# Optimization experiments

Hardware: AMD Instinct MI355X
Metric: run time of the kernel (lower is better)

## Reference

```python
import jax, jax.numpy as jnp
import numpy as np

N = 16_777_216
EPS = 1e-6  # keep probabilities strictly inside (0,1) so log terms are finite


def setup_inputs() -> dict:
    key = jax.random.key(0)
    k1, k2 = jax.random.split(key)
    inputs = jax.random.uniform(k1, (N,), dtype=jnp.float32, minval=EPS, maxval=1.0 - EPS)
    targets = jax.random.randint(k2, (N,), 0, 2, dtype=jnp.int32)
    return {"inputs": inputs, "targets": targets}


def reference(inputs, targets):
    t = targets.astype(inputs.dtype)
    # multiplier = 1.0 + 0.1 per element with prediction > 0.5 but label 0
    # (vectorized equivalent of the original per-element Python loop)
    count = jnp.sum(((inputs > 0.5) & (targets == 0)).astype(inputs.dtype))
    multiplier = 1.0 + 0.1 * count
    # element-wise BCE: -(t*log(p) + (1-t)*log(1-p))
    loss = -(t * jnp.log(inputs) + (1.0 - t) * jnp.log(1.0 - inputs))
    return loss.mean() * multiplier
```

## Files before the change

kernel.cpp:

```cpp
#include <hip/hip_runtime.h>


#define N_ELEM  16777216
#define N_VEC4  (N_ELEM / 4)
#define BLOCKS  2048
#define TPB     256
#define NTHREAD (BLOCKS * TPB)
#define NITER   (N_VEC4 / NTHREAD)

typedef float f4v __attribute__((ext_vector_type(4)));
typedef int   i4v __attribute__((ext_vector_type(4)));


__global__ __launch_bounds__(TPB, 4) void cl_reduce(
    const f4v* __restrict__ p4,
    const i4v* __restrict__ t4,
    float2*    __restrict__ part)
{
    const int tid = blockIdx.x * TPB + threadIdx.x;

    f4v p[NITER];
    i4v t[NITER];
    #pragma unroll
    for (int j = 0; j < NITER; ++j) {
        p[j] = __builtin_nontemporal_load(&p4[tid + j * NTHREAD]);
        t[j] = __builtin_nontemporal_load(&t4[tid + j * NTHREAD]);
    }
    __builtin_amdgcn_sched_barrier(0);

    float        lsum = 0.0f;
    unsigned int lcnt = 0u;
    #pragma unroll
    for (int j = 0; j < NITER; ++j) {
        lsum += __logf(t[j][0] ? p[j][0] : 1.0f - p[j][0]);
        lsum += __logf(t[j][1] ? p[j][1] : 1.0f - p[j][1]);
        lsum += __logf(t[j][2] ? p[j][2] : 1.0f - p[j][2]);
        lsum += __logf(t[j][3] ? p[j][3] : 1.0f - p[j][3]);
        lcnt += (unsigned int)((p[j][0] > 0.5f) & (t[j][0] == 0));
        lcnt += (unsigned int)((p[j][1] > 0.5f) & (t[j][1] == 0));
        lcnt += (unsigned int)((p[j][2] > 0.5f) & (t[j][2] == 0));
        lcnt += (unsigned int)((p[j][3] > 0.5f) & (t[j][3] == 0));
    }
    lsum = -lsum;

    #pragma unroll
    for (int off = 32; off > 0; off >>= 1) {
        lsum += __shfl_down(lsum, off);
        lcnt += __shfl_down(lcnt, off);
    }

    __shared__ float        s_sum[4];
    __shared__ unsigned int s_cnt[4];
    const int wave = threadIdx.x >> 6;
    const int lane = threadIdx.x & 63;
    if (lane == 0) { s_sum[wave] = lsum; s_cnt[wave] = lcnt; }
    __syncthreads();
    if (threadIdx.x == 0) {
        float2 v;
        v.x = s_sum[0] + s_sum[1] + s_sum[2] + s_sum[3];
        v.y = __uint_as_float(s_cnt[0] + s_cnt[1] + s_cnt[2] + s_cnt[3]);
        part[blockIdx.x] = v;
    }
}

__global__ __launch_bounds__(TPB) void cl_final(
    const float2* __restrict__ part,
    float*        __restrict__ out)
{
    double       s = 0.0;
    unsigned int c = 0u;
    #pragma unroll
    for (int j = 0; j < BLOCKS / TPB; ++j) {
        const float2 v = part[threadIdx.x + j * TPB];
        s += (double)v.x;
        c += __float_as_uint(v.y);
    }
    #pragma unroll
    for (int off = 32; off > 0; off >>= 1) {
        s += __shfl_down(s, off);
        c += __shfl_down(c, off);
    }
    __shared__ double       ss[4];
    __shared__ unsigned int sc[4];
    const int wave = threadIdx.x >> 6;
    const int lane = threadIdx.x & 63;
    if (lane == 0) { ss[wave] = s; sc[wave] = c; }
    __syncthreads();
    if (threadIdx.x == 0) {
        const double       tot = ss[0] + ss[1] + ss[2] + ss[3];
        const unsigned int tc  = sc[0] + sc[1] + sc[2] + sc[3];
        out[0] = (float)((tot * (1.0 / (double)N_ELEM)) * (1.0 + 0.1 * (double)tc));
    }
}

extern "C" void kernel_launch(void* const* d_in, const int* in_sizes, int n_in,
                              void* d_out, int out_size, void* d_ws, size_t ws_size,
                              hipStream_t stream) {
    const f4v* p4  = (const f4v*)d_in[0];
    const i4v* t4  = (const i4v*)d_in[1];
    float*     out = (float*)d_out;
    float2*    part = (float2*)d_ws;

    cl_reduce<<<BLOCKS, TPB, 0, stream>>>(p4, t4, part);
    cl_final<<<1, TPB, 0, stream>>>(part, out);
}
```

Measured before the change: 34.41 us.

## Fuse final reduction into main kernel via last-block atomic ticket

Replaces the separate single-block finalisation kernel with a last-block-done pattern: each block atomically stores its packed partial sum and count, then increments a global ticket counter, and the block that draws the final ticket performs the cross-block reduction and writes the output. This removes the second kernel launch and its inter-kernel gap, but adds a memset of the counter on each call plus atomic traffic. Memory ordering relies on relaxed atomics and an explicit vmcnt wait rather than release/acquire fences.

After: 44.28 us. 28.7% more time.

```diff
diff --git a/kernel.cpp b/kernel.cpp
--- a/kernel.cpp
+++ b/kernel.cpp
@@ -11,11 +11,14 @@
 typedef float f4v __attribute__((ext_vector_type(4)));
 typedef int   i4v __attribute__((ext_vector_type(4)));
 
+#define WS_CTR_OFF 16384
 
-__global__ __launch_bounds__(TPB, 4) void cl_reduce(
+__global__ __launch_bounds__(TPB, 4) void cl_fused(
     const f4v* __restrict__ p4,
     const i4v* __restrict__ t4,
-    float2*    __restrict__ part)
+    unsigned long long* __restrict__ part,
+    unsigned int*       __restrict__ ctr,
+    float*              __restrict__ out)
 {
     const int tid = blockIdx.x * TPB + threadIdx.x;
 
@@ -51,45 +54,50 @@
 
     __shared__ float        s_sum[4];
     __shared__ unsigned int s_cnt[4];
+    __shared__ unsigned int s_ticket;
     const int wave = threadIdx.x >> 6;
     const int lane = threadIdx.x & 63;
     if (lane == 0) { s_sum[wave] = lsum; s_cnt[wave] = lcnt; }
     __syncthreads();
+
     if (threadIdx.x == 0) {
-        float2 v;
-        v.x = s_sum[0] + s_sum[1] + s_sum[2] + s_sum[3];
-        v.y = __uint_as_float(s_cnt[0] + s_cnt[1] + s_cnt[2] + s_cnt[3]);
-        part[blockIdx.x] = v;
+        const float        bs = s_sum[0] + s_sum[1] + s_sum[2] + s_sum[3];
+        const unsigned int bc = s_cnt[0] + s_cnt[1] + s_cnt[2] + s_cnt[3];
+        const unsigned long long pk =
+            ((unsigned long long)bc << 32) | (unsigned long long)__float_as_uint(bs);
+        __hip_atomic_store(&part[blockIdx.x], pk,
+                           __ATOMIC_RELAXED, __HIP_MEMORY_SCOPE_AGENT);
+        asm volatile("s_waitcnt vmcnt(0)" ::: "memory");
+        s_ticket = __hip_atomic_fetch_add(ctr, 1u,
+                                          __ATOMIC_RELAXED, __HIP_MEMORY_SCOPE_AGENT);
     }
-}
+    __syncthreads();
 
-__global__ __launch_bounds__(TPB) void cl_final(
-    const float2* __restrict__ part,
-    float*        __restrict__ out)
-{
-    double       s = 0.0;
-    unsigned int c = 0u;
-    #pragma unroll
-    for (int j = 0; j < BLOCKS / TPB; ++j) {
-        const float2 v = part[threadIdx.x + j * TPB];
-        s += (double)v.x;
-        c += __float_as_uint(v.y);
-    }
-    #pragma unroll
-    for (int off = 32; off > 0; off >>= 1) {
-        s += __shfl_down(s, off);
-        c += __shfl_down(c, off);
-    }
-    __shared__ double       ss[4];
-    __shared__ unsigned int sc[4];
-    const int wave = threadIdx.x >> 6;
-    const int lane = threadIdx.x & 63;
-    if (lane == 0) { ss[wave] = s; sc[wave] = c; }
-    __syncthreads();
-    if (threadIdx.x == 0) {
-        const double       tot = ss[0] + ss[1] + ss[2] + ss[3];
-        const unsigned int tc  = sc[0] + sc[1] + sc[2] + sc[3];
-        out[0] = (float)((tot * (1.0 / (double)N_ELEM)) * (1.0 + 0.1 * (double)tc));
+    if (s_ticket == BLOCKS - 1) {
+        double       s = 0.0;
+        unsigned int c = 0u;
+        #pragma unroll
+        for (int j = 0; j < BLOCKS / TPB; ++j) {
+            const unsigned long long v =
+                __hip_atomic_load(&part[threadIdx.x + j * TPB],
+                                  __ATOMIC_RELAXED, __HIP_MEMORY_SCOPE_AGENT);
+            s += (double)__uint_as_float((unsigned int)(v & 0xffffffffull));
+            c += (unsigned int)(v >> 32);
+        }
+        #pragma unroll
+        for (int off = 32; off > 0; off >>= 1) {
+            s += __shfl_down(s, off);
+            c += __shfl_down(c, off);
+        }
+        __shared__ double       fs[4];
+        __shared__ unsigned int fc[4];
+        if (lane == 0) { fs[wave] = s; fc[wave] = c; }
+        __syncthreads();
+        if (threadIdx.x == 0) {
+            const double       tot = fs[0] + fs[1] + fs[2] + fs[3];
+            const unsigned int tc  = fc[0] + fc[1] + fc[2] + fc[3];
+            out[0] = (float)((tot * (1.0 / (double)N_ELEM)) * (1.0 + 0.1 * (double)tc));
+        }
     }
 }
 
@@ -99,8 +107,11 @@
     const f4v* p4  = (const f4v*)d_in[0];
     const i4v* t4  = (const i4v*)d_in[1];
     float*     out = (float*)d_out;
-    float2*    part = (float2*)d_ws;
 
-    cl_reduce<<<BLOCKS, TPB, 0, stream>>>(p4, t4, part);
-    cl_final<<<1, TPB, 0, stream>>>(part, out);
+    unsigned long long* part = (unsigned long long*)d_ws;
+    unsigned int*       ctr  = (unsigned int*)((char*)d_ws + WS_CTR_OFF);
+
+    hipMemsetAsync(ctr, 0, sizeof(unsigned int), stream);
+
+    cl_fused<<<BLOCKS, TPB, 0, stream>>>(p4, t4, part, ctr, out);
 }
```
